# Kernel optimization log

Measured on AMD Instinct MI355X. Metric: run time of the kernel, lower is better.

## Reference

```python
import jax, jax.numpy as jnp
import numpy as np

BS, S, D, H = 2, 2048, 1024, 16
DH = D // H  # 64


def setup_inputs() -> dict:
    key = jax.random.key(0)
    k1, k2, k3 = jax.random.split(key, 3)
    x = jax.random.normal(k1, (BS, S, D), dtype=jnp.float32)
    w_qkv = jax.random.normal(k2, (D, H, 3 * DH), dtype=jnp.float32) * (D ** -0.5)
    b_qkv = jnp.zeros((H, 3 * DH), dtype=jnp.float32)
    w_out = jax.random.normal(k3, (H, DH, D), dtype=jnp.float32) * (D ** -0.5)
    b_out = jnp.zeros((D,), dtype=jnp.float32)
    return {"x": x, "w_qkv": w_qkv, "b_qkv": b_qkv, "w_out": w_out, "b_out": b_out}


def reference(x, w_qkv, b_qkv, w_out, b_out):
    dtype = x.dtype
    # QKV projection: DenseGeneral(features=(H, 3*DH)) -> [B, S, H, 3*DH]
    qkv = jnp.einsum("bsd,dhf->bshf", x, w_qkv) + b_qkv
    q, k, v = jnp.split(qkv, 3, axis=-1)  # each [B, S, H, DH]

    scale = DH ** -0.5
    q = (q * scale).astype(jnp.float32)
    k = k.astype(jnp.float32)
    # Full causal attention with fp32 scores (as in original)
    weights = jnp.einsum("bqhd,bkhd->bhqk", q, k)  # [B, H, S, S]
    causal = jnp.tril(jnp.ones((S, S), dtype=bool))[None, None, :, :]
    weights = jnp.where(causal, weights, jnp.finfo(jnp.float32).min)
    weights = jax.nn.softmax(weights, axis=-1).astype(dtype)
    attn = jnp.einsum("bhqk,bkhd->bqhd", weights, v).astype(dtype)

    # Output projection: DenseGeneral(D, axis=(-2, -1))
    out = jnp.einsum("bqhd,hdo->bqo", attn, w_out) + b_out
    return out
```

## Files before the change

kernel.cpp:

```cpp
#include <hip/hip_runtime.h>
#include <hip/hip_bf16.h>
#include <stdint.h>

#define NBS 2
#define SEQ 2048
#define DMODEL 1024
#define NH 16
#define DHEAD 64
#define MROWS (NBS*SEQ)
#define NQKV (NH*3*DHEAD)

typedef __bf16 bf16;
typedef __bf16 bf16x8 __attribute__((ext_vector_type(8)));
typedef float f32x4 __attribute__((ext_vector_type(4)));
typedef float f32x16 __attribute__((ext_vector_type(16)));
typedef unsigned int u32x2 __attribute__((ext_vector_type(2)));

#define LOG2E 1.44269504088896f
#define QSCALE (0.125f * LOG2E)

static __device__ __forceinline__ void gload_lds16(const bf16* g, bf16* l) {
    __builtin_amdgcn_global_load_lds(
        (const __attribute__((address_space(1))) uint32_t*)g,
        (__attribute__((address_space(3))) uint32_t*)l, 16, 0, 0);
}

static __device__ __forceinline__ bf16x8 ld_b8(const bf16* p) {
    return __builtin_bit_cast(bf16x8, *(const uint4*)p);
}

static __device__ __forceinline__ uint32_t pk_bf16(float lo, float hi) {
    unsigned short l = __builtin_bit_cast(unsigned short, (bf16)lo);
    unsigned short h = __builtin_bit_cast(unsigned short, (bf16)hi);
    return ((uint32_t)h << 16) | (uint32_t)l;
}

static __device__ __forceinline__ u32x2 lane_swap32(uint32_t a, uint32_t b, int lane) {
#if __has_builtin(__builtin_amdgcn_permlane32_swap)
    return __builtin_amdgcn_permlane32_swap(a, b, false, false);
#else
    uint32_t sa = __shfl_xor(a, 32), sb = __shfl_xor(b, 32);
    u32x2 r;
    r.x = (lane >= 32) ? sb : a;
    r.y = (lane >= 32) ? b : sa;
    return r;
#endif
}


__global__ void k_cvt(const float* __restrict__ in, bf16* __restrict__ out, int n4) {
    int i = blockIdx.x * blockDim.x + threadIdx.x;
    if (i < n4) {
        float4 v = ((const float4*)in)[i];
        ushort4 o;
        o.x = __builtin_bit_cast(unsigned short, (bf16)v.x);
        o.y = __builtin_bit_cast(unsigned short, (bf16)v.y);
        o.z = __builtin_bit_cast(unsigned short, (bf16)v.z);
        o.w = __builtin_bit_cast(unsigned short, (bf16)v.w);
        ((ushort4*)out)[i] = o;
    }
}

__global__ void k_tcvt(const float* __restrict__ in, bf16* __restrict__ out, int R, int C) {
    __shared__ float t[32][33];
    int tx = threadIdx.x, ty = threadIdx.y;
    int r0 = blockIdx.y * 32, c0 = blockIdx.x * 32;
#pragma unroll
    for (int i = 0; i < 4; i++)
        t[ty + i*8][tx] = in[(size_t)(r0 + ty + i*8) * C + (c0 + tx)];
    __syncthreads();
#pragma unroll
    for (int i = 0; i < 4; i++)
        out[(size_t)(c0 + ty + i*8) * R + (r0 + tx)] = (bf16)t[tx][ty + i*8];
}

__global__ void k_tcvt_qkv(const float* __restrict__ in, bf16* __restrict__ out) {
    __shared__ float t[32][33];
    int tx = threadIdx.x, ty = threadIdx.y;
    int r0 = blockIdx.y * 32, c0 = blockIdx.x * 32;
#pragma unroll
    for (int i = 0; i < 4; i++)
        t[ty + i*8][tx] = in[(size_t)(r0 + ty + i*8) * NQKV + (c0 + tx)];
    __syncthreads();
#pragma unroll
    for (int i = 0; i < 4; i++) {
        int c = c0 + ty + i*8;
        int h = c / 192, f = c % 192;
        int cperm = ((f >> 6) << 10) + (h << 6) + (f & 63);
        out[(size_t)cperm * DMODEL + (r0 + tx)] = (bf16)t[tx][ty + i*8];
    }
}

template<int KD>
static __device__ __forceinline__ void gemm_tile(
        const bf16* __restrict__ A, const bf16* __restrict__ Bt,
        bf16* As, bf16* Bs, f32x4 acc[4][4], int tile_m, int tile_n) {
    int tid = threadIdx.x;
    int wave = tid >> 6, lane = tid & 63;
    int wr = wave >> 1, wc = wave & 1;
    int g = lane >> 4, r = lane & 15;
    int srow = lane >> 2, schunk = (lane & 3) * 8;

#pragma unroll
    for (int m = 0; m < 4; m++)
#pragma unroll
        for (int n = 0; n < 4; n++)
            acc[m][n] = (f32x4){0.f, 0.f, 0.f, 0.f};

    for (int k0 = 0; k0 < KD; k0 += 32) {
#pragma unroll
        for (int i = 0; i < 2; i++) {
            int ii = wave + i * 4;
            gload_lds16(A  + (size_t)(tile_m + ii*16 + srow) * KD + k0 + schunk, As + ii*512);
            gload_lds16(Bt + (size_t)(tile_n + ii*16 + srow) * KD + k0 + schunk, Bs + ii*512);
        }
        __syncthreads();
        bf16x8 af[4], bfr[4];
#pragma unroll
        for (int m = 0; m < 4; m++) af[m]  = *(const bf16x8*)(As + (wr*64 + m*16 + r)*32 + g*8);
#pragma unroll
        for (int n = 0; n < 4; n++) bfr[n] = *(const bf16x8*)(Bs + (wc*64 + n*16 + r)*32 + g*8);
#pragma unroll
        for (int m = 0; m < 4; m++)
#pragma unroll
            for (int n = 0; n < 4; n++)
                acc[m][n] = __builtin_amdgcn_mfma_f32_16x16x32_bf16(af[m], bfr[n], acc[m][n], 0, 0, 0);
        __syncthreads();
    }
}

__global__ __launch_bounds__(256) void k_gemm_qkv(
        const bf16* __restrict__ A, const bf16* __restrict__ Bt,
        const float* __restrict__ bias,
        bf16* __restrict__ Q, bf16* __restrict__ Kp, bf16* __restrict__ Vt) {
    __shared__ __align__(16) bf16 As[128*32];
    __shared__ __align__(16) bf16 Bs[128*32];
    f32x4 acc[4][4];
    int tile_m = blockIdx.y * 128, tile_n = blockIdx.x * 128;
    gemm_tile<DMODEL>(A, Bt, As, Bs, acc, tile_m, tile_n);

    int wave = threadIdx.x >> 6, lane = threadIdx.x & 63;
    int wr = wave >> 1, wc = wave & 1, g = lane >> 4, r = lane & 15;
#pragma unroll
    for (int m = 0; m < 4; m++) {
#pragma unroll
        for (int n = 0; n < 4; n++) {
            int col = tile_n + wc*64 + n*16 + r;
            int kind = col >> 10;
            int h = (col >> 6) & 15;
            int d = col & 63;
            float bv = bias[h*192 + (kind << 6) + d];
#pragma unroll
            for (int j = 0; j < 4; j++) {
                int row = tile_m + wr*64 + m*16 + g*4 + j;
                int b = row >> 11, s = row & 2047;
                float v = acc[m][n][j] + bv;
                if (kind == 0) {
                    Q[(((size_t)(b*NH + h)) * SEQ + s) * DHEAD + d] = (bf16)(v * QSCALE);
                } else if (kind == 1) {
                    Kp[(((size_t)(b*NH + h)) * SEQ + s) * DHEAD + d] = (bf16)v;
                } else {
                    Vt[(((size_t)(b*NH + h)) * DHEAD + d) * SEQ + s] = (bf16)v;
                }
            }
        }
    }
}

__global__ __launch_bounds__(256) void k_gemm_out(
        const bf16* __restrict__ A, const bf16* __restrict__ Bt,
        const float* __restrict__ bias, float* __restrict__ out) {
    __shared__ __align__(16) bf16 As[128*32];
    __shared__ __align__(16) bf16 Bs[128*32];
    f32x4 acc[4][4];
    int tile_m = blockIdx.y * 128, tile_n = blockIdx.x * 128;
    gemm_tile<DMODEL>(A, Bt, As, Bs, acc, tile_m, tile_n);

    int wave = threadIdx.x >> 6, lane = threadIdx.x & 63;
    int wr = wave >> 1, wc = wave & 1, g = lane >> 4, r = lane & 15;
#pragma unroll
    for (int m = 0; m < 4; m++) {
#pragma unroll
        for (int n = 0; n < 4; n++) {
            int col = tile_n + wc*64 + n*16 + r;
            float bv = bias[col];
#pragma unroll
            for (int j = 0; j < 4; j++) {
                int row = tile_m + wr*64 + m*16 + g*4 + j;
                out[(size_t)row * DMODEL + col] = acc[m][n][j] + bv;
            }
        }
    }
}

#define QBLK 128
#define KVB 64

static __device__ __forceinline__ void attn_tile_body(
        const bf16* Ks, const bf16* VsT,
        const bf16x8 qa2[4], f32x16 o32[2], float& l_part,
        int kv0, int qb, int qrow, int l31, int hi, int lane) {
    const f32x16 z16 = {0,0,0,0,0,0,0,0,0,0,0,0,0,0,0,0};
    f32x16 st[2];
    st[0] = z16; st[1] = z16;
    __builtin_amdgcn_s_setprio(1);
#pragma unroll
    for (int c = 0; c < 4; c++) {
#pragma unroll
        for (int rb = 0; rb < 2; rb++) {
            bf16x8 kf = ld_b8(&Ks[(rb*32 + l31)*72 + c*16 + hi*8]);
            st[rb] = __builtin_amdgcn_mfma_f32_32x32x16_bf16(kf, qa2[c], st[rb], 0, 0, 0);
        }
    }
    __builtin_amdgcn_s_setprio(0);

    bf16x8 vf[2][4];
#pragma unroll
    for (int dblk = 0; dblk < 2; dblk++)
#pragma unroll
        for (int c = 0; c < 4; c++)
            vf[dblk][c] = ld_b8(&VsT[(dblk*32 + l31)*72 + c*16 + hi*8]);

    bool needm = (kv0 + KVB - 1) > qb;
    float l4[4] = {0.f, 0.f, 0.f, 0.f};
#pragma unroll
    for (int rb = 0; rb < 2; rb++) {
#pragma unroll
        for (int reg = 0; reg < 16; reg++) {
            float e = __builtin_amdgcn_exp2f(st[rb][reg]);
            if (needm) {
                int kv = kv0 + rb*32 + (reg & 3) + 8*(reg >> 2) + 4*hi;
                if (kv > qrow) e = 0.f;
            }
            l4[reg & 3] += e;
            st[rb][reg] = e;
        }
    }
    l_part += (l4[0] + l4[1]) + (l4[2] + l4[3]);

    bf16x8 pa[4];
#pragma unroll
    for (int c = 0; c < 4; c++) {
        const f32x16& pp = st[c >> 1];
        const int base = (c & 1) * 8;
        uint32_t a0 = pk_bf16(pp[base+0], pp[base+1]);
        uint32_t a1 = pk_bf16(pp[base+2], pp[base+3]);
        uint32_t b0 = pk_bf16(pp[base+4], pp[base+5]);
        uint32_t b1 = pk_bf16(pp[base+6], pp[base+7]);
        u32x2 s0 = lane_swap32(a0, b0, lane);
        u32x2 s1 = lane_swap32(a1, b1, lane);
        uint4 fr = {s0.x, s1.x, s0.y, s1.y};
        pa[c] = __builtin_bit_cast(bf16x8, fr);
    }

    __builtin_amdgcn_s_setprio(1);
#pragma unroll
    for (int dblk = 0; dblk < 2; dblk++)
#pragma unroll
        for (int c = 0; c < 4; c++)
            o32[dblk] = __builtin_amdgcn_mfma_f32_32x32x16_bf16(pa[c], vf[dblk][c], o32[dblk], 0, 0, 0);
    __builtin_amdgcn_s_setprio(0);
}

__device__ const int8_t JQC[32]  = {10,10, 4, 0, 15,15, 3, 1,  9, 9, 7, 2, 13,14, 7, 5,
                                    14,14,11, 5, 15, 8,11, 6,  8,12,12, 6, 13,13,11,12};
__device__ const int8_t JT0[32]  = { 0,11, 0, 0,  0,11, 0, 0,  0,10, 0, 0,  0, 0, 8, 0,
                                    10,20, 0, 6, 22, 0, 8, 0,  9, 0, 9, 7, 10,19,16,18};
__device__ const int8_t JT1[32]  = {11,22,10, 2, 11,22, 8, 4, 10,20, 8, 6, 10,10,16, 6,
                                    20,30, 8,12, 32, 9,16, 7, 18, 9,18,14, 19,28,24,26};
__device__ const int8_t JSEG[32] = { 0, 1, 0, 0,  0, 1, 0, 0,  0, 1, 0, 0,  0, 0, 1, 0,
                                     1, 2, 0, 1,  2, 0, 1, 0,  1, 0, 1, 1,  1, 2, 2, 2};

__global__ __launch_bounds__(256) void k_attn_split(
        const bf16* __restrict__ Q, const bf16* __restrict__ K,
        const bf16* __restrict__ Vt,
        bf16* __restrict__ Op0, bf16* __restrict__ Op1, bf16* __restrict__ Op2,
        float* __restrict__ Lp0, float* __restrict__ Lp1, float* __restrict__ Lp2) {
    int scu = blockIdx.x;
    int bh = scu >> 3, slot = scu & 7;
    int j = slot * 4 + blockIdx.y;
    int qc  = JQC[j];
    int t0  = JT0[j];
    int t1  = JT1[j];
    int seg = JSEG[j];
    int q0 = qc * QBLK;
    int tid = threadIdx.x, wave = tid >> 6, lane = tid & 63;
    int l31 = lane & 31, hi = lane >> 5;

    __shared__ __align__(16) bf16 Ks[2][KVB*72];
    __shared__ __align__(16) bf16 VsT[2][KVB*72];

    const bf16* Kg = K  + (size_t)bh * SEQ * DHEAD;
    const bf16* Vg = Vt + (size_t)bh * DHEAD * SEQ;

    int qb = q0 + wave * 32;
    int qrow = qb + l31;

    const bf16* qrow_p = Q + ((size_t)bh * SEQ + qrow) * DHEAD;
    bf16x8 qa2[4];
#pragma unroll
    for (int c = 0; c < 4; c++) qa2[c] = ld_b8(qrow_p + c*16 + hi*8);

    const f32x16 z16 = {0,0,0,0,0,0,0,0,0,0,0,0,0,0,0,0};
    f32x16 o32[2];
    o32[0] = z16; o32[1] = z16;
    float l_part = 0.f;

    int qmax_wave = qb + 31;

    int krow0 = tid >> 3, kseg0 = (tid & 7) * 8;
    int krow1 = krow0 + 32;
    int vd0 = tid >> 3, vseg0 = (tid & 7) * 8;
    int vd1 = vd0 + 32;

    bf16x8 kreg[2], vreg[2];
    {
        int kvs = t0 * KVB;
        kreg[0] = ld_b8(Kg + (size_t)(kvs + krow0) * DHEAD + kseg0);
        kreg[1] = ld_b8(Kg + (size_t)(kvs + krow1) * DHEAD + kseg0);
        vreg[0] = ld_b8(Vg + (size_t)vd0 * SEQ + kvs + vseg0);
        vreg[1] = ld_b8(Vg + (size_t)vd1 * SEQ + kvs + vseg0);
    }

    int cur = 0;
    for (int t = t0; t < t1; t++) {
        int kv0 = t * KVB;
        *(uint4*)&Ks[cur][krow0*72 + kseg0]  = __builtin_bit_cast(uint4, kreg[0]);
        *(uint4*)&Ks[cur][krow1*72 + kseg0]  = __builtin_bit_cast(uint4, kreg[1]);
        *(uint4*)&VsT[cur][vd0*72 + vseg0]   = __builtin_bit_cast(uint4, vreg[0]);
        *(uint4*)&VsT[cur][vd1*72 + vseg0]   = __builtin_bit_cast(uint4, vreg[1]);
        __syncthreads();

        if (t + 1 < t1) {
            int kv1 = kv0 + KVB;
            kreg[0] = ld_b8(Kg + (size_t)(kv1 + krow0) * DHEAD + kseg0);
            kreg[1] = ld_b8(Kg + (size_t)(kv1 + krow1) * DHEAD + kseg0);
            vreg[0] = ld_b8(Vg + (size_t)vd0 * SEQ + kv1 + vseg0);
            vreg[1] = ld_b8(Vg + (size_t)vd1 * SEQ + kv1 + vseg0);
        }

        if (kv0 <= qmax_wave)
            attn_tile_body(Ks[cur], VsT[cur], qa2, o32, l_part,
                           kv0, qb, qrow, l31, hi, lane);
        cur ^= 1;
    }

    bf16* Op; float* Lp; size_t obase; int lbase;
    if (seg == 0)      { Op = Op0; Lp = Lp0; obase = ((size_t)bh*2048 + q0) * 64;          lbase = bh*2048 + q0; }
    else if (seg == 1) { Op = Op1; Lp = Lp1; obase = ((size_t)bh*1408 + (qc-5)*128) * 64;  lbase = bh*1408 + (qc-5)*128; }
    else               { Op = Op2; Lp = Lp2; obase = ((size_t)bh*640  + (qc-11)*128) * 64; lbase = bh*640  + (qc-11)*128; }

    l_part += __shfl_xor(l_part, 32);
    if (hi == 0)
        Lp[lbase + wave*32 + l31] = l_part;

#pragma unroll
    for (int reg = 0; reg < 16; reg++) {
        int qr = (reg & 3) + 8*(reg >> 2) + 4*hi;
        size_t base = obase + (size_t)(wave*32 + qr) * 64 + l31;
        Op[base]      = (bf16)o32[0][reg];
        Op[base + 32] = (bf16)o32[1][reg];
    }
}

__global__ __launch_bounds__(256) void k_merge(
        const bf16* __restrict__ Op0, const bf16* __restrict__ Op1,
        const bf16* __restrict__ Op2,
        const float* __restrict__ Lp0, const float* __restrict__ Lp1,
        const float* __restrict__ Lp2,
        bf16* __restrict__ Oa) {
    int g = blockIdx.x * 256 + threadIdx.x;
    int dseg = g & 7;
    int s = (g >> 3) & 2047;
    int bh = g >> 14;
    int qc = s >> 7;
    int sl = s & 127;

    size_t r0 = ((size_t)bh * 2048 + s) * 64 + dseg*8;
    bf16x8 p0 = ld_b8(Op0 + r0);
    float l = Lp0[bh*2048 + s];
    float acc[8];
#pragma unroll
    for (int i = 0; i < 8; i++) acc[i] = (float)p0[i];

    if (qc >= 5) {
        size_t r1 = ((size_t)bh * 1408 + (qc-5)*128 + sl) * 64 + dseg*8;
        bf16x8 p1 = ld_b8(Op1 + r1);
        l += Lp1[bh*1408 + (qc-5)*128 + sl];
#pragma unroll
        for (int i = 0; i < 8; i++) acc[i] += (float)p1[i];
        if (qc >= 11) {
            size_t r2 = ((size_t)bh * 640 + (qc-11)*128 + sl) * 64 + dseg*8;
            bf16x8 p2 = ld_b8(Op2 + r2);
            l += Lp2[bh*640 + (qc-11)*128 + sl];
#pragma unroll
            for (int i = 0; i < 8; i++) acc[i] += (float)p2[i];
        }
    }

    float inv = 1.0f / l;
    bf16x8 r;
#pragma unroll
    for (int i = 0; i < 8; i++) r[i] = (bf16)(acc[i] * inv);
    int b = bh >> 4, h = bh & 15;
    *(uint4*)&Oa[(((size_t)b * SEQ + s) * NH + h) * DHEAD + dseg*8] =
        __builtin_bit_cast(uint4, r);
}

__global__ __launch_bounds__(256) void k_attn(
        const bf16* __restrict__ Q, const bf16* __restrict__ K,
        const bf16* __restrict__ Vt, bf16* __restrict__ O) {
    int bh = blockIdx.y;
    int qc = (bh >= 16) ? (15 - (int)blockIdx.x) : (int)blockIdx.x;
    int q0 = qc * QBLK;
    int tid = threadIdx.x, wave = tid >> 6, lane = tid & 63;
    int l31 = lane & 31, hi = lane >> 5;

    __shared__ __align__(16) bf16 Ks[2][KVB*72];
    __shared__ __align__(16) bf16 VsT[2][KVB*72];

    const bf16* Kg = K  + (size_t)bh * SEQ * DHEAD;
    const bf16* Vg = Vt + (size_t)bh * DHEAD * SEQ;

    int qb = q0 + wave * 32;
    int qrow = qb + l31;

    const bf16* qrow_p = Q + ((size_t)bh * SEQ + qrow) * DHEAD;
    bf16x8 qa2[4];
#pragma unroll
    for (int c = 0; c < 4; c++) qa2[c] = ld_b8(qrow_p + c*16 + hi*8);

    const f32x16 z16 = {0,0,0,0,0,0,0,0,0,0,0,0,0,0,0,0};
    f32x16 o32[2];
    o32[0] = z16; o32[1] = z16;
    float l_part = 0.f;

    int nt = 2*qc + 2;
    int qmax_wave = qb + 31;

    int krow0 = tid >> 3, kseg0 = (tid & 7) * 8;
    int krow1 = krow0 + 32;
    int vd0 = tid >> 3, vseg0 = (tid & 7) * 8;
    int vd1 = vd0 + 32;

    bf16x8 kreg[2], vreg[2];
    kreg[0] = ld_b8(Kg + (size_t)krow0 * DHEAD + kseg0);
    kreg[1] = ld_b8(Kg + (size_t)krow1 * DHEAD + kseg0);
    vreg[0] = ld_b8(Vg + (size_t)vd0 * SEQ + vseg0);
    vreg[1] = ld_b8(Vg + (size_t)vd1 * SEQ + vseg0);

    int cur = 0;
    for (int t = 0; t < nt; t++) {
        int kv0 = t * KVB;
        *(uint4*)&Ks[cur][krow0*72 + kseg0]  = __builtin_bit_cast(uint4, kreg[0]);
        *(uint4*)&Ks[cur][krow1*72 + kseg0]  = __builtin_bit_cast(uint4, kreg[1]);
        *(uint4*)&VsT[cur][vd0*72 + vseg0]   = __builtin_bit_cast(uint4, vreg[0]);
        *(uint4*)&VsT[cur][vd1*72 + vseg0]   = __builtin_bit_cast(uint4, vreg[1]);
        __syncthreads();

        if (t + 1 < nt) {
            int kv1 = kv0 + KVB;
            kreg[0] = ld_b8(Kg + (size_t)(kv1 + krow0) * DHEAD + kseg0);
            kreg[1] = ld_b8(Kg + (size_t)(kv1 + krow1) * DHEAD + kseg0);
            vreg[0] = ld_b8(Vg + (size_t)vd0 * SEQ + kv1 + vseg0);
            vreg[1] = ld_b8(Vg + (size_t)vd1 * SEQ + kv1 + vseg0);
        }

        if (kv0 <= qmax_wave)
            attn_tile_body(Ks[cur], VsT[cur], qa2, o32, l_part,
                           kv0, qb, qrow, l31, hi, lane);
        cur ^= 1;
    }

    l_part += __shfl_xor(l_part, 32);
    float linv = 1.0f / l_part;

    float lrv[16];
#pragma unroll
    for (int reg = 0; reg < 16; reg++) {
        int qr = (reg & 3) + 8*(reg >> 2) + 4*hi;
        lrv[reg] = __shfl(linv, qr);
    }

    int b = bh >> 4, h = bh & 15;
#pragma unroll
    for (int reg = 0; reg < 16; reg++) {
        int qr = (reg & 3) + 8*(reg >> 2) + 4*hi;
        int srow = q0 + wave*32 + qr;
        size_t base = (((size_t)b * SEQ + srow) * NH + h) * DHEAD + l31;
        O[base]      = (bf16)(o32[0][reg] * lrv[reg]);
        O[base + 32] = (bf16)(o32[1][reg] * lrv[reg]);
    }
}


extern "C" void kernel_launch(void* const* d_in, const int* in_sizes, int n_in,
                              void* d_out, int out_size, void* d_ws, size_t ws_size,
                              hipStream_t stream) {
    const float* x     = (const float*)d_in[0];
    const float* w_qkv = (const float*)d_in[1];
    const float* b_qkv = (const float*)d_in[2];
    const float* w_out = (const float*)d_in[3];
    const float* b_out = (const float*)d_in[4];
    float* out = (float*)d_out;

    char* ws = (char*)d_ws;
    bf16* xb   = (bf16*)(ws);
    bf16* wqkT = (bf16*)(ws + 8388608);
    bf16* woT  = (bf16*)(ws + 14680064);
    bf16* qb   = (bf16*)(ws + 16777216);
    bf16* kb   = (bf16*)(ws + 25165824);
    bf16* vb   = (bf16*)(ws + 33554432);
    bf16* Op0  = (bf16*)(ws + 41943040);
    bf16* Op1  = (bf16*)(ws + 50331648);
    bf16* Op2  = (bf16*)(ws + 56098816);
    float* Lp0 = (float*)(ws + 8388608);
    float* Lp1 = (float*)(ws + 8388608 + 262144);
    float* Lp2 = (float*)(ws + 8388608 + 524288);
    const size_t WS_NEED = 58720256;
    bf16* attn = xb;

    k_cvt<<<(MROWS*DMODEL/4 + 255)/256, 256, 0, stream>>>(x, xb, MROWS*DMODEL/4);
    dim3 tb(32, 8);
    k_tcvt_qkv<<<dim3(NQKV/32, DMODEL/32), tb, 0, stream>>>(w_qkv, wqkT);
    k_tcvt<<<dim3(DMODEL/32, DMODEL/32), tb, 0, stream>>>(w_out, woT, DMODEL, DMODEL);

    k_gemm_qkv<<<dim3(NQKV/128, MROWS/128), 256, 0, stream>>>(xb, wqkT, b_qkv, qb, kb, vb);

    if (ws_size >= WS_NEED) {
        k_attn_split<<<dim3(256, 4), 256, 0, stream>>>(qb, kb, vb,
                                                       Op0, Op1, Op2, Lp0, Lp1, Lp2);
        k_merge<<<(NBS*NH*SEQ*DHEAD/8)/256, 256, 0, stream>>>(Op0, Op1, Op2,
                                                              Lp0, Lp1, Lp2, attn);
    } else {
        k_attn<<<dim3(SEQ/QBLK, NBS*NH), 256, 0, stream>>>(qb, kb, vb, attn);
    }

    k_gemm_out<<<dim3(DMODEL/128, MROWS/128), 256, 0, stream>>>(attn, woT, b_out, out);
}
```

Before: 125.5 us.

## Swizzle LDS layouts, widen GEMM K-step, compute softmax row sums via MFMA

Replaces padded LDS layouts (stride 72) in the attention kernels with unpadded XOR-swizzled layouts, and does the same for the GEMM tiles while doubling the K-step to 64 per barrier. The softmax denominator is now accumulated with an extra MFMA against a ones vector instead of per-lane VALU adds and cross-lane shuffles, so the row sum lands in the same register layout as the output. The aim is fewer bank conflicts, half as many barriers in the GEMM, and less VALU and shuffle work in attention. The cost is more LDS per GEMM block and four extra MFMAs per tile, and the row sums now come from bf16-rounded probabilities.

```diff
diff --git a/kernel.cpp b/kernel.cpp
--- a/kernel.cpp
+++ b/kernel.cpp
@@ -99,7 +99,8 @@
     int wave = tid >> 6, lane = tid & 63;
     int wr = wave >> 1, wc = wave & 1;
     int g = lane >> 4, r = lane & 15;
-    int srow = lane >> 2, schunk = (lane & 3) * 8;
+    int grow = lane >> 3;
+    int gc8 = (lane & 7) ^ grow;
 
 #pragma unroll
     for (int m = 0; m < 4; m++)
@@ -107,24 +108,31 @@
         for (int n = 0; n < 4; n++)
             acc[m][n] = (f32x4){0.f, 0.f, 0.f, 0.f};
 
-    for (int k0 = 0; k0 < KD; k0 += 32) {
-#pragma unroll
-        for (int i = 0; i < 2; i++) {
+    int sw = (r & 7) << 3;
+
+    for (int k0 = 0; k0 < KD; k0 += 64) {
+#pragma unroll
+        for (int i = 0; i < 4; i++) {
             int ii = wave + i * 4;
-            gload_lds16(A  + (size_t)(tile_m + ii*16 + srow) * KD + k0 + schunk, As + ii*512);
-            gload_lds16(Bt + (size_t)(tile_n + ii*16 + srow) * KD + k0 + schunk, Bs + ii*512);
+            gload_lds16(A  + (size_t)(tile_m + ii*8 + grow) * KD + k0 + gc8*8, As + ii*512);
+            gload_lds16(Bt + (size_t)(tile_n + ii*8 + grow) * KD + k0 + gc8*8, Bs + ii*512);
         }
         __syncthreads();
-        bf16x8 af[4], bfr[4];
-#pragma unroll
-        for (int m = 0; m < 4; m++) af[m]  = *(const bf16x8*)(As + (wr*64 + m*16 + r)*32 + g*8);
-#pragma unroll
-        for (int n = 0; n < 4; n++) bfr[n] = *(const bf16x8*)(Bs + (wc*64 + n*16 + r)*32 + g*8);
-#pragma unroll
-        for (int m = 0; m < 4; m++)
+#pragma unroll
+        for (int kk = 0; kk < 2; kk++) {
+            bf16x8 af[4], bfr[4];
+#pragma unroll
+            for (int m = 0; m < 4; m++)
+                af[m] = ld_b8(As + ((((wr*64 + m*16 + r)*64) + kk*32 + g*8) ^ sw));
 #pragma unroll
             for (int n = 0; n < 4; n++)
-                acc[m][n] = __builtin_amdgcn_mfma_f32_16x16x32_bf16(af[m], bfr[n], acc[m][n], 0, 0, 0);
+                bfr[n] = ld_b8(Bs + ((((wc*64 + n*16 + r)*64) + kk*32 + g*8) ^ sw));
+#pragma unroll
+            for (int m = 0; m < 4; m++)
+#pragma unroll
+                for (int n = 0; n < 4; n++)
+                    acc[m][n] = __builtin_amdgcn_mfma_f32_16x16x32_bf16(af[m], bfr[n], acc[m][n], 0, 0, 0);
+        }
         __syncthreads();
     }
 }
@@ -133,8 +141,8 @@
         const bf16* __restrict__ A, const bf16* __restrict__ Bt,
         const float* __restrict__ bias,
         bf16* __restrict__ Q, bf16* __restrict__ Kp, bf16* __restrict__ Vt) {
-    __shared__ __align__(16) bf16 As[128*32];
-    __shared__ __align__(16) bf16 Bs[128*32];
+    __shared__ __align__(16) bf16 As[128*64];
+    __shared__ __align__(16) bf16 Bs[128*64];
     f32x4 acc[4][4];
     int tile_m = blockIdx.y * 128, tile_n = blockIdx.x * 128;
     gemm_tile<DMODEL>(A, Bt, As, Bs, acc, tile_m, tile_n);
@@ -170,8 +178,8 @@
 __global__ __launch_bounds__(256) void k_gemm_out(
         const bf16* __restrict__ A, const bf16* __restrict__ Bt,
         const float* __restrict__ bias, float* __restrict__ out) {
-    __shared__ __align__(16) bf16 As[128*32];
-    __shared__ __align__(16) bf16 Bs[128*32];
+    __shared__ __align__(16) bf16 As[128*64];
+    __shared__ __align__(16) bf16 Bs[128*64];
     f32x4 acc[4][4];
     int tile_m = blockIdx.y * 128, tile_n = blockIdx.x * 128;
     gemm_tile<DMODEL>(A, Bt, As, Bs, acc, tile_m, tile_n);
@@ -198,17 +206,19 @@
 
 static __device__ __forceinline__ void attn_tile_body(
         const bf16* Ks, const bf16* VsT,
-        const bf16x8 qa2[4], f32x16 o32[2], float& l_part,
+        const bf16x8 qa2[4], const bf16x8& ones,
+        f32x16 o32[2], f32x16& acc_l,
         int kv0, int qb, int qrow, int l31, int hi, int lane) {
     const f32x16 z16 = {0,0,0,0,0,0,0,0,0,0,0,0,0,0,0,0};
+    int sw = (l31 & 7) << 3;
     f32x16 st[2];
     st[0] = z16; st[1] = z16;
     __builtin_amdgcn_s_setprio(1);
 #pragma unroll
-    for (int c = 0; c < 4; c++) {
-#pragma unroll
-        for (int rb = 0; rb < 2; rb++) {
-            bf16x8 kf = ld_b8(&Ks[(rb*32 + l31)*72 + c*16 + hi*8]);
+    for (int rb = 0; rb < 2; rb++) {
+#pragma unroll
+        for (int c = 0; c < 4; c++) {
+            bf16x8 kf = ld_b8(Ks + ((((rb*32 + l31)*64) + c*16 + hi*8) ^ sw));
             st[rb] = __builtin_amdgcn_mfma_f32_32x32x16_bf16(kf, qa2[c], st[rb], 0, 0, 0);
         }
     }
@@ -219,10 +229,9 @@
     for (int dblk = 0; dblk < 2; dblk++)
 #pragma unroll
         for (int c = 0; c < 4; c++)
-            vf[dblk][c] = ld_b8(&VsT[(dblk*32 + l31)*72 + c*16 + hi*8]);
+            vf[dblk][c] = ld_b8(VsT + ((((dblk*32 + l31)*64) + c*16 + hi*8) ^ sw));
 
     bool needm = (kv0 + KVB - 1) > qb;
-    float l4[4] = {0.f, 0.f, 0.f, 0.f};
 #pragma unroll
     for (int rb = 0; rb < 2; rb++) {
 #pragma unroll
@@ -232,11 +241,9 @@
                 int kv = kv0 + rb*32 + (reg & 3) + 8*(reg >> 2) + 4*hi;
                 if (kv > qrow) e = 0.f;
             }
-            l4[reg & 3] += e;
             st[rb][reg] = e;
         }
     }
-    l_part += (l4[0] + l4[1]) + (l4[2] + l4[3]);
 
     bf16x8 pa[4];
 #pragma unroll
@@ -259,6 +266,9 @@
 #pragma unroll
         for (int c = 0; c < 4; c++)
             o32[dblk] = __builtin_amdgcn_mfma_f32_32x32x16_bf16(pa[c], vf[dblk][c], o32[dblk], 0, 0, 0);
+#pragma unroll
+    for (int c = 0; c < 4; c++)
+        acc_l = __builtin_amdgcn_mfma_f32_32x32x16_bf16(pa[c], ones, acc_l, 0, 0, 0);
     __builtin_amdgcn_s_setprio(0);
 }
 
@@ -287,8 +297,8 @@
     int tid = threadIdx.x, wave = tid >> 6, lane = tid & 63;
     int l31 = lane & 31, hi = lane >> 5;
 
-    __shared__ __align__(16) bf16 Ks[2][KVB*72];
-    __shared__ __align__(16) bf16 VsT[2][KVB*72];
+    __shared__ __align__(16) bf16 Ks[2][KVB*64];
+    __shared__ __align__(16) bf16 VsT[2][KVB*64];
 
     const bf16* Kg = K  + (size_t)bh * SEQ * DHEAD;
     const bf16* Vg = Vt + (size_t)bh * DHEAD * SEQ;
@@ -301,46 +311,49 @@
 #pragma unroll
     for (int c = 0; c < 4; c++) qa2[c] = ld_b8(qrow_p + c*16 + hi*8);
 
+    bf16x8 ones;
+#pragma unroll
+    for (int c = 0; c < 8; c++) ones[c] = (bf16)1.0f;
+
     const f32x16 z16 = {0,0,0,0,0,0,0,0,0,0,0,0,0,0,0,0};
-    f32x16 o32[2];
-    o32[0] = z16; o32[1] = z16;
-    float l_part = 0.f;
+    f32x16 o32[2], acc_l;
+    o32[0] = z16; o32[1] = z16; acc_l = z16;
 
     int qmax_wave = qb + 31;
 
-    int krow0 = tid >> 3, kseg0 = (tid & 7) * 8;
-    int krow1 = krow0 + 32;
-    int vd0 = tid >> 3, vseg0 = (tid & 7) * 8;
-    int vd1 = vd0 + 32;
+    int srow = tid >> 3, sc8 = tid & 7;
+    int sw_st = (srow & 7) << 3;
+    int wK0 = ((srow*64)      + sc8*8) ^ sw_st;
+    int wK1 = (((srow+32)*64) + sc8*8) ^ sw_st;
 
     bf16x8 kreg[2], vreg[2];
     {
         int kvs = t0 * KVB;
-        kreg[0] = ld_b8(Kg + (size_t)(kvs + krow0) * DHEAD + kseg0);
-        kreg[1] = ld_b8(Kg + (size_t)(kvs + krow1) * DHEAD + kseg0);
-        vreg[0] = ld_b8(Vg + (size_t)vd0 * SEQ + kvs + vseg0);
-        vreg[1] = ld_b8(Vg + (size_t)vd1 * SEQ + kvs + vseg0);
+        kreg[0] = ld_b8(Kg + (size_t)(kvs + srow)      * DHEAD + sc8*8);
+        kreg[1] = ld_b8(Kg + (size_t)(kvs + srow + 32) * DHEAD + sc8*8);
+        vreg[0] = ld_b8(Vg + (size_t)srow      * SEQ + kvs + sc8*8);
+        vreg[1] = ld_b8(Vg + (size_t)(srow+32) * SEQ + kvs + sc8*8);
     }
 
     int cur = 0;
     for (int t = t0; t < t1; t++) {
         int kv0 = t * KVB;
-        *(uint4*)&Ks[cur][krow0*72 + kseg0]  = __builtin_bit_cast(uint4, kreg[0]);
-        *(uint4*)&Ks[cur][krow1*72 + kseg0]  = __builtin_bit_cast(uint4, kreg[1]);
-        *(uint4*)&VsT[cur][vd0*72 + vseg0]   = __builtin_bit_cast(uint4, vreg[0]);
-        *(uint4*)&VsT[cur][vd1*72 + vseg0]   = __builtin_bit_cast(uint4, vreg[1]);
+        *(uint4*)&Ks[cur][wK0]  = __builtin_bit_cast(uint4, kreg[0]);
+        *(uint4*)&Ks[cur][wK1]  = __builtin_bit_cast(uint4, kreg[1]);
+        *(uint4*)&VsT[cur][wK0] = __builtin_bit_cast(uint4, vreg[0]);
+        *(uint4*)&VsT[cur][wK1] = __builtin_bit_cast(uint4, vreg[1]);
         __syncthreads();
 
         if (t + 1 < t1) {
             int kv1 = kv0 + KVB;
-            kreg[0] = ld_b8(Kg + (size_t)(kv1 + krow0) * DHEAD + kseg0);
-            kreg[1] = ld_b8(Kg + (size_t)(kv1 + krow1) * DHEAD + kseg0);
-            vreg[0] = ld_b8(Vg + (size_t)vd0 * SEQ + kv1 + vseg0);
-            vreg[1] = ld_b8(Vg + (size_t)vd1 * SEQ + kv1 + vseg0);
+            kreg[0] = ld_b8(Kg + (size_t)(kv1 + srow)      * DHEAD + sc8*8);
+            kreg[1] = ld_b8(Kg + (size_t)(kv1 + srow + 32) * DHEAD + sc8*8);
+            vreg[0] = ld_b8(Vg + (size_t)srow      * SEQ + kv1 + sc8*8);
+            vreg[1] = ld_b8(Vg + (size_t)(srow+32) * SEQ + kv1 + sc8*8);
         }
 
         if (kv0 <= qmax_wave)
-            attn_tile_body(Ks[cur], VsT[cur], qa2, o32, l_part,
+            attn_tile_body(Ks[cur], VsT[cur], qa2, ones, o32, acc_l,
                            kv0, qb, qrow, l31, hi, lane);
         cur ^= 1;
     }
@@ -350,9 +363,13 @@
     else if (seg == 1) { Op = Op1; Lp = Lp1; obase = ((size_t)bh*1408 + (qc-5)*128) * 64;  lbase = bh*1408 + (qc-5)*128; }
     else               { Op = Op2; Lp = Lp2; obase = ((size_t)bh*640  + (qc-11)*128) * 64; lbase = bh*640  + (qc-11)*128; }
 
-    l_part += __shfl_xor(l_part, 32);
-    if (hi == 0)
-        Lp[lbase + wave*32 + l31] = l_part;
+    if (l31 == 0) {
+#pragma unroll
+        for (int reg = 0; reg < 16; reg++) {
+            int qr = (reg & 3) + 8*(reg >> 2) + 4*hi;
+            Lp[lbase + wave*32 + qr] = acc_l[reg];
+        }
+    }
 
 #pragma unroll
     for (int reg = 0; reg < 16; reg++) {
@@ -416,8 +433,8 @@
     int tid = threadIdx.x, wave = tid >> 6, lane = tid & 63;
     int l31 = lane & 31, hi = lane >> 5;
 
-    __shared__ __align__(16) bf16 Ks[2][KVB*72];
-    __shared__ __align__(16) bf16 VsT[2][KVB*72];
+    __shared__ __align__(16) bf16 Ks[2][KVB*64];
+    __shared__ __align__(16) bf16 VsT[2][KVB*64];
 
     const bf16* Kg = K  + (size_t)bh * SEQ * DHEAD;
     const bf16* Vg = Vt + (size_t)bh * DHEAD * SEQ;
@@ -430,66 +447,60 @@
 #pragma unroll
     for (int c = 0; c < 4; c++) qa2[c] = ld_b8(qrow_p + c*16 + hi*8);
 
+    bf16x8 ones;
+#pragma unroll
+    for (int c = 0; c < 8; c++) ones[c] = (bf16)1.0f;
+
     const f32x16 z16 = {0,0,0,0,0,0,0,0,0,0,0,0,0,0,0,0};
-    f32x16 o32[2];
-    o32[0] = z16; o32[1] = z16;
-    float l_part = 0.f;
+    f32x16 o32[2], acc_l;
+    o32[0] = z16; o32[1] = z16; acc_l = z16;
 
     int nt = 2*qc + 2;
     int qmax_wave = qb + 31;
 
-    int krow0 = tid >> 3, kseg0 = (tid & 7) * 8;
-    int krow1 = krow0 + 32;
-    int vd0 = tid >> 3, vseg0 = (tid & 7) * 8;
-    int vd1 = vd0 + 32;
+    int srow = tid >> 3, sc8 = tid & 7;
+    int sw_st = (srow & 7) << 3;
+    int wK0 = ((srow*64)      + sc8*8) ^ sw_st;
+    int wK1 = (((srow+32)*64) + sc8*8) ^ sw_st;
 
     bf16x8 kreg[2], vreg[2];
-    kreg[0] = ld_b8(Kg + (size_t)krow0 * DHEAD + kseg0);
-    kreg[1] = ld_b8(Kg + (size_t)krow1 * DHEAD + kseg0);
-    vreg[0] = ld_b8(Vg + (size_t)vd0 * SEQ + vseg0);
-    vreg[1] = ld_b8(Vg + (size_t)vd1 * SEQ + vseg0);
+    kreg[0] = ld_b8(Kg + (size_t)srow      * DHEAD + sc8*8);
+    kreg[1] = ld_b8(Kg + (size_t)(srow+32) * DHEAD + sc8*8);
+    vreg[0] = ld_b8(Vg + (size_t)srow      * SEQ + sc8*8);
+    vreg[1] = ld_b8(Vg + (size_t)(srow+32) * SEQ + sc8*8);
 
     int cur = 0;
     for (int t = 0; t < nt; t++) {
         int kv0 = t * KVB;
-        *(uint4*)&Ks[cur][krow0*72 + kseg0]  = __builtin_bit_cast(uint4, kreg[0]);
-        *(uint4*)&Ks[cur][krow1*72 + kseg0]  = __builtin_bit_cast(uint4, kreg[1]);
-        *(uint4*)&VsT[cur][vd0*72 + vseg0]   = __builtin_bit_cast(uint4, vreg[0]);
-        *(uint4*)&VsT[cur][vd1*72 + vseg0]   = __builtin_bit_cast(uint4, vreg[1]);
+        *(uint4*)&Ks[cur][wK0]  = __builtin_bit_cast(uint4, kreg[0]);
+        *(uint4*)&Ks[cur][wK1]  = __builtin_bit_cast(uint4, kreg[1]);
+        *(uint4*)&VsT[cur][wK0] = __builtin_bit_cast(uint4, vreg[0]);
+        *(uint4*)&VsT[cur][wK1] = __builtin_bit_cast(uint4, vreg[1]);
         __syncthreads();
 
         if (t + 1 < nt) {
             int kv1 = kv0 + KVB;
-            kreg[0] = ld_b8(Kg + (size_t)(kv1 + krow0) * DHEAD + kseg0);
-            kreg[1] = ld_b8(Kg + (size_t)(kv1 + krow1) * DHEAD + kseg0);
-            vreg[0] = ld_b8(Vg + (size_t)vd0 * SEQ + kv1 + vseg0);
-            vreg[1] = ld_b8(Vg + (size_t)vd1 * SEQ + kv1 + vseg0);
+            kreg[0] = ld_b8(Kg + (size_t)(kv1 + srow)      * DHEAD + sc8*8);
+            kreg[1] = ld_b8(Kg + (size_t)(kv1 + srow + 32) * DHEAD + sc8*8);
+            vreg[0] = ld_b8(Vg + (size_t)srow      * SEQ + kv1 + sc8*8);
+            vreg[1] = ld_b8(Vg + (size_t)(srow+32) * SEQ + kv1 + sc8*8);
         }
 
         if (kv0 <= qmax_wave)
-            attn_tile_body(Ks[cur], VsT[cur], qa2, o32, l_part,
+            attn_tile_body(Ks[cur], VsT[cur], qa2, ones, o32, acc_l,
                            kv0, qb, qrow, l31, hi, lane);
         cur ^= 1;
     }
 
-    l_part += __shfl_xor(l_part, 32);
-    float linv = 1.0f / l_part;
-
-    float lrv[16];
+    int b = bh >> 4, h = bh & 15;
 #pragma unroll
     for (int reg = 0; reg < 16; reg++) {
         int qr = (reg & 3) + 8*(reg >> 2) + 4*hi;
-        lrv[reg] = __shfl(linv, qr);
-    }
-
-    int b = bh >> 4, h = bh & 15;
-#pragma unroll
-    for (int reg = 0; reg < 16; reg++) {
-        int qr = (reg & 3) + 8*(reg >> 2) + 4*hi;
-        int srow = q0 + wave*32 + qr;
-        size_t base = (((size_t)b * SEQ + srow) * NH + h) * DHEAD + l31;
-        O[base]      = (bf16)(o32[0][reg] * lrv[reg]);
-        O[base + 32] = (bf16)(o32[1][reg] * lrv[reg]);
+        int srow2 = q0 + wave*32 + qr;
+        float linv = 1.0f / acc_l[reg];
+        size_t base = (((size_t)b * SEQ + srow2) * NH + h) * DHEAD + l31;
+        O[base]      = (bf16)(o32[0][reg] * linv);
+        O[base + 32] = (bf16)(o32[1][reg] * linv);
     }
 }
 
```

After: 140.8 us. 1.12x slower.
